# Kernel optimization log

Hardware: AMD Instinct MI355X
Metric: run time of the kernel (lower is better)

Reference implementation:

```python
import jax, jax.numpy as jnp
import numpy as np

D_MODEL = 1024
NUM_EXPERTS = 16
TOP_K = 2
CAPACITY_FACTOR = 1.25
SINKHORN_ITERS = 3
AUX_LOSS_WEIGHT = 0.01


def setup_inputs() -> dict:
    key = jax.random.key(0)
    ks = jax.random.split(key, 6)
    d, e, h = D_MODEL, NUM_EXPERTS, 4 * D_MODEL
    sd = 1.0 / np.sqrt(d)
    sh = 1.0 / np.sqrt(h)
    return {
        "x": jax.random.normal(ks[0], (4, 2048, d), dtype=jnp.float32),
        "W_router": jax.random.uniform(ks[1], (d, e), jnp.float32, -sd, sd),
        "W1": jax.random.uniform(ks[2], (e, d, h), jnp.float32, -sd, sd),
        "b1": jax.random.uniform(ks[3], (e, h), jnp.float32, -sd, sd),
        "W2": jax.random.uniform(ks[4], (e, h, d), jnp.float32, -sh, sh),
        "b2": jax.random.uniform(ks[5], (e, d), jnp.float32, -sh, sh),
    }


def _moe_forward(x, W_router, W1, b1, W2, b2):
    B, S, D = x.shape
    E, K = NUM_EXPERTS, TOP_K
    N = B * S
    capacity = max(int(N * CAPACITY_FACTOR / E), K)  # static python int

    xf = x.reshape(N, D)
    router_logits = xf @ W_router                      # [N, E]
    probs = jax.nn.softmax(router_logits, axis=-1)
    # Sinkhorn balancing (as in source: row-normalize, col-normalize, rescale)
    for _ in range(SINKHORN_ITERS):
        probs = probs / probs.sum(axis=-1, keepdims=True)
        probs = probs / probs.sum(axis=0, keepdims=True)
        probs = probs * (N / E)

    weights, indices = jax.lax.top_k(probs, K)         # [N, K]
    weights = weights / weights.sum(axis=-1, keepdims=True)

    # --- dispatch: sequential slot allocation in (t, k) order ---
    flat_e = indices.reshape(-1)                       # [N*K]
    onehot = (flat_e[:, None] == jnp.arange(E)[None, :]).astype(jnp.int32)  # [N*K, E]
    # position of each dispatch within its expert = count of earlier same-expert entries
    pos = (jnp.cumsum(onehot, axis=0) * onehot).sum(-1) - 1                  # [N*K]
    mask = pos < capacity                              # dispatch_mask flattened
    total_counts = onehot.sum(0)                       # [E]
    token_counts = jnp.minimum(total_counts, capacity)

    safe_pos = jnp.where(mask, pos, 0)
    flat_idx = jnp.where(mask, flat_e * capacity + safe_pos, E * capacity)
    x_rep = jnp.repeat(xf, K, axis=0)                  # [N*K, D], (t,k) order
    buf = jnp.zeros((E * capacity + 1, D), dtype=x.dtype)
    buf = buf.at[flat_idx].set(x_rep)
    expert_input = buf[: E * capacity].reshape(E, capacity, D)

    # --- per-expert MLP (exact GELU, as torch.nn.GELU default) ---
    h = jnp.einsum('ecd,edf->ecf', expert_input, W1) + b1[:, None, :]
    h = jax.nn.gelu(h, approximate=False)
    expert_output = jnp.einsum('ecf,efd->ecd', h, W2) + b2[:, None, :]  # [E, cap, D]

    # --- weighted gather-combine ---
    gathered = expert_output[flat_e, safe_pos]         # [N*K, D]
    w = (weights.reshape(-1) * mask.astype(weights.dtype))[:, None]
    y = (gathered * w).reshape(N, K, D).sum(axis=1).reshape(B, S, D)

    aux_loss = AUX_LOSS_WEIGHT * E * (
        probs.mean(axis=0) * (token_counts.astype(probs.dtype) / N)
    ).sum()
    return y, aux_loss


def reference(x, W_router, W1, b1, W2, b2):
    return _moe_forward(x, W_router, W1, b1, W2, b2)
```

## Files before the change

kernel.cpp:

```cpp
#include <hip/hip_runtime.h>
#include <hip/hip_bf16.h>
#include <math.h>

#define NTOK 8192
#define DM   1024
#define NE   16
#define HD   4096
#define CAP  640
#define NCHUNK 64

typedef float f32x4 __attribute__((ext_vector_type(4)));
typedef _Float16 f16x8 __attribute__((ext_vector_type(8)));
typedef _Float16 f16x4 __attribute__((ext_vector_type(4)));

__device__ __forceinline__ void gload16(const void* g, void* l) {
  __builtin_amdgcn_global_load_lds(
      (const __attribute__((address_space(1))) unsigned int*)g,
      (__attribute__((address_space(3))) unsigned int*)l, 16, 0, 0);
}

__device__ __forceinline__ float gelu_fast(float v) {
  float v2 = v * v;
  float z2n = v * fmaf(-0.07135481627f, v2, -1.595769122f);
  float e = __expf(z2n);
  return v / (1.0f + e);
}

__global__ __launch_bounds__(256) void k_router(const float* __restrict__ x,
                                                const float* __restrict__ Wr,
                                                float* __restrict__ probs,
                                                float* __restrict__ pout) {
  int wave = threadIdx.x >> 6, lane = threadIdx.x & 63;
  int tok = blockIdx.x * 4 + wave;
  const float* xr = x + (size_t)tok * DM;
  float acc[NE];
#pragma unroll
  for (int e = 0; e < NE; ++e) acc[e] = 0.f;
  for (int d = lane; d < DM; d += 64) {
    float xv = xr[d];
    const float* w = Wr + (size_t)d * NE;
#pragma unroll
    for (int e = 0; e < NE; ++e) acc[e] = fmaf(xv, w[e], acc[e]);
  }
#pragma unroll
  for (int off = 32; off >= 1; off >>= 1) {
#pragma unroll
    for (int e = 0; e < NE; ++e) acc[e] += __shfl_xor(acc[e], off, 64);
  }
  float m = acc[0];
#pragma unroll
  for (int e = 1; e < NE; ++e) m = fmaxf(m, acc[e]);
  float s = 0.f;
#pragma unroll
  for (int e = 0; e < NE; ++e) { acc[e] = expf(acc[e] - m); s += acc[e]; }
  float inv = 1.0f / s;
#pragma unroll
  for (int e = 0; e < NE; ++e) acc[e] *= inv;
  if (lane < NE) probs[(size_t)tok * NE + lane] = acc[lane];
  __shared__ float wsum[4][NE];
  if (lane == 0) {
#pragma unroll
    for (int e = 0; e < NE; ++e) wsum[wave][e] = acc[e];
  }
  __syncthreads();
  if (threadIdx.x < NE)
    pout[blockIdx.x * NE + threadIdx.x] =
        wsum[0][threadIdx.x] + wsum[1][threadIdx.x] + wsum[2][threadIdx.x] + wsum[3][threadIdx.x];
}

__global__ __launch_bounds__(256) void k_sink(float* __restrict__ probs,
                                              const float* __restrict__ pin,
                                              float* __restrict__ pout) {
  __shared__ float csinv[NE];
  int tid = threadIdx.x;
  if (tid < NE) {
    float s = 0.f;
#pragma unroll
    for (int b = 0; b < 32; ++b) s += pin[b * NE + tid];
    csinv[tid] = 512.0f / s;
  }
  __syncthreads();
  int tok = blockIdx.x * 256 + tid;
  float* row = probs + (size_t)tok * NE;
  float p[NE]; float rs = 0.f;
#pragma unroll
  for (int e = 0; e < NE; ++e) { p[e] = row[e] * csinv[e]; rs += p[e]; }
  float rinv = 1.0f / rs;
#pragma unroll
  for (int e = 0; e < NE; ++e) { p[e] *= rinv; row[e] = p[e]; }
#pragma unroll
  for (int off = 32; off >= 1; off >>= 1) {
#pragma unroll
    for (int e = 0; e < NE; ++e) p[e] += __shfl_xor(p[e], off, 64);
  }
  __shared__ float wsum[4][NE];
  int lane = tid & 63, wave = tid >> 6;
  if (lane == 0) {
#pragma unroll
    for (int e = 0; e < NE; ++e) wsum[wave][e] = p[e];
  }
  __syncthreads();
  if (tid < NE)
    pout[blockIdx.x * NE + tid] =
        wsum[0][tid] + wsum[1][tid] + wsum[2][tid] + wsum[3][tid];
}

__global__ __launch_bounds__(256) void k_sink3(const float* __restrict__ probs,
                                               const float* __restrict__ pin,
                                               int* __restrict__ eidx,
                                               float* __restrict__ ew,
                                               int* __restrict__ cnt) {
  __shared__ float csinv[NE];
  __shared__ int h0[NE], h1[NE];
  int tid = threadIdx.x;
  if (tid < NE) {
    float s = 0.f;
#pragma unroll
    for (int b = 0; b < 32; ++b) s += pin[b * NE + tid];
    csinv[tid] = 512.0f / s;
    h0[tid] = 0; h1[tid] = 0;
  }
  __syncthreads();
  int tok = blockIdx.x * 256 + tid;
  const float* row = probs + (size_t)tok * NE;
  float v0 = -1e30f, v1 = -1e30f; int e0 = 0, e1 = 0;
#pragma unroll
  for (int e = 0; e < NE; ++e) {
    float v = row[e] * csinv[e];
    if (v > v0) { v1 = v0; e1 = e0; v0 = v; e0 = e; }
    else if (v > v1) { v1 = v; e1 = e; }
  }
  float s = v0 + v1;
  eidx[tok * 2] = e0; eidx[tok * 2 + 1] = e1;
  ew[tok * 2] = v0 / s; ew[tok * 2 + 1] = v1 / s;
  int* hh = (tid < 128) ? h0 : h1;
  atomicAdd(&hh[e0], 1);
  atomicAdd(&hh[e1], 1);
  __syncthreads();
  if (tid < NE) cnt[(2 * blockIdx.x) * NE + tid] = h0[tid];
  else if (tid >= 32 && tid < 32 + NE) cnt[(2 * blockIdx.x + 1) * NE + (tid - 32)] = h1[tid - 32];
}

__global__ __launch_bounds__(64) void k_prefix(const int* __restrict__ cnt,
                                               int* __restrict__ base,
                                               int* __restrict__ counts,
                                               float* __restrict__ aux) {
  __shared__ int tot[NE];
  int e = threadIdx.x;
  if (e < NE) {
    int run = 0;
    for (int c = 0; c < NCHUNK; ++c) {
      base[c * NE + e] = run;
      run += cnt[c * NE + e];
    }
    counts[e] = run;
    tot[e] = min(run, CAP);
  }
  __syncthreads();
  if (e == 0) {
    int s = 0;
#pragma unroll
    for (int i = 0; i < NE; ++i) s += tot[i];
    *aux = 0.01f * (float)s / (float)NTOK;
  }
}

__global__ __launch_bounds__(256) void k_assign(const int* __restrict__ eidx,
                                                const int* __restrict__ base,
                                                int* __restrict__ slot_tok,
                                                int* __restrict__ tok2slot) {
  __shared__ int wcnt[4][NE];
  __shared__ int cbase[NE];
  int tid = threadIdx.x, c = blockIdx.x, lane = tid & 63, wave = tid >> 6;
  int i = c * 256 + tid;
  int myE = eidx[i];
  if (tid < NE) cbase[tid] = base[c * NE + tid];
  int mypre = 0;
#pragma unroll
  for (int e = 0; e < NE; ++e) {
    unsigned long long m = __ballot(myE == e);
    if (myE == e) mypre = __popcll(m & ((1ull << lane) - 1ull));
    if (lane == 0) wcnt[wave][e] = __popcll(m);
  }
  __syncthreads();
  int pre = 0;
  for (int w = 0; w < wave; ++w) pre += wcnt[w][myE];
  int pos = cbase[myE] + pre + mypre;
  if (pos < CAP) {
    slot_tok[myE * CAP + pos] = i >> 1;
    tok2slot[i] = myE * CAP + pos;
  } else {
    tok2slot[i] = -1;
  }
}

__global__ __launch_bounds__(256) void k_gather(const float* __restrict__ x,
                                                const int* __restrict__ slot_tok,
                                                _Float16* __restrict__ xg) {
  int row = blockIdx.x;
  int tok = slot_tok[row];
  int t = threadIdx.x;
  f16x4 h;
  if (tok >= 0) {
    float4 v = *(const float4*)(x + (size_t)tok * DM + t * 4);
    h[0] = (_Float16)v.x; h[1] = (_Float16)v.y; h[2] = (_Float16)v.z; h[3] = (_Float16)v.w;
  } else {
    h[0] = (_Float16)0.f; h[1] = (_Float16)0.f; h[2] = (_Float16)0.f; h[3] = (_Float16)0.f;
  }
  *(f16x4*)(xg + (size_t)row * DM + t * 4) = h;
}


__device__ __forceinline__ void stage_tileA128(const _Float16* gbase, int ld, int k0,
                                               _Float16* lds, int w, int lane) {
#pragma unroll
  for (int i = 0; i < 4; ++i) {
    int ci = (w * 4 + i) * 64 + lane;
    int row = ci >> 3, c = ci & 7;
    int cs = c ^ (row & 7);
    gload16(gbase + (size_t)row * ld + k0 + cs * 8, lds + (w * 4 + i) * 512);
  }
}

__device__ __forceinline__ void loadB8(const float* gb, int ld, int k0, int tid, float4* L) {
  int nq = tid & 31, kc = tid >> 5;
  const float* p = gb + (size_t)(k0 + kc * 8) * ld + nq * 4;
#pragma unroll
  for (int j = 0; j < 8; ++j) L[j] = *(const float4*)(p + (size_t)j * ld);
}

__device__ __forceinline__ void writeB(_Float16* Bs, int tid, const float4* L) {
  int nq = tid & 31, kc = tid >> 5;
#pragma unroll
  for (int i = 0; i < 4; ++i) {
    int n = nq * 4 + i;
    int pos = kc ^ ((n ^ (n >> 2)) & 7);
    f16x8 v;
#pragma unroll
    for (int j = 0; j < 8; ++j) {
      float f = (i == 0) ? L[j].x : (i == 1) ? L[j].y : (i == 2) ? L[j].z : L[j].w;
      v[j] = (_Float16)f;
    }
    *(f16x8*)(Bs + n * 64 + pos * 8) = v;
  }
}

#define MFMA_PHASE(Ac, Bs)                                                         \
  _Pragma("unroll")                                                                \
  for (int ks = 0; ks < 2; ++ks) {                                                 \
    f16x8 af[4], bf[4];                                                            \
    _Pragma("unroll")                                                              \
    for (int m = 0; m < 4; ++m) {                                                  \
      int row = wr * 64 + m * 16 + lr;                                             \
      int cs = (ks * 4 + kg) ^ (row & 7);                                          \
      af[m] = *(const f16x8*)((Ac) + row * 64 + cs * 8);                           \
    }                                                                              \
    _Pragma("unroll")                                                              \
    for (int n = 0; n < 4; ++n) {                                                  \
      int row = wc * 64 + n * 16 + lr;                                             \
      int cs = (ks * 4 + kg) ^ ((row ^ (row >> 2)) & 7);                           \
      bf[n] = *(const f16x8*)((Bs) + row * 64 + cs * 8);                           \
    }                                                                              \
    __builtin_amdgcn_s_setprio(1);                                                 \
    _Pragma("unroll")                                                              \
    for (int m = 0; m < 4; ++m)                                                    \
      _Pragma("unroll")                                                            \
      for (int n = 0; n < 4; ++n)                                                  \
        acc[m][n] = __builtin_amdgcn_mfma_f32_16x16x32_f16(af[m], bf[n], acc[m][n], 0, 0, 0); \
    __builtin_amdgcn_s_setprio(0);                                                 \
  }

#define ASYNC_K_LOOP(NT, AB, ALD, BB, BLD, KBASE)                                  \
  {                                                                                \
    stage_tileA128((AB), (ALD), (KBASE), As0, w, lane);                            \
    loadB8((BB), (BLD), (KBASE), tid, L);                                          \
    asm volatile("s_waitcnt vmcnt(0)" ::: "memory");                               \
    __builtin_amdgcn_s_barrier();                                                  \
    __builtin_amdgcn_sched_barrier(0);                                             \
    for (int t = 0; t < (NT); ++t) {                                               \
      const _Float16* Ac = (t & 1) ? As1 : As0;                                    \
      _Float16* An = (t & 1) ? As0 : As1;                                          \
      writeB(Bs, tid, L);                                                          \
      if (t + 1 < (NT)) {                                                          \
        stage_tileA128((AB), (ALD), (KBASE) + (t + 1) * 64, An, w, lane);          \
        loadB8((BB), (BLD), (KBASE) + (t + 1) * 64, tid, L);                       \
      }                                                                            \
      asm volatile("s_waitcnt lgkmcnt(0)" ::: "memory");                           \
      __builtin_amdgcn_s_barrier();                                                \
      __builtin_amdgcn_sched_barrier(0);                                           \
      MFMA_PHASE(Ac, Bs);                                                          \
      __builtin_amdgcn_sched_barrier(0);                                           \
      if (t + 1 < (NT)) { asm volatile("s_waitcnt vmcnt(8)" ::: "memory"); }       \
      else              { asm volatile("s_waitcnt vmcnt(0)" ::: "memory"); }       \
      __builtin_amdgcn_s_barrier();                                                \
      __builtin_amdgcn_sched_barrier(0);                                           \
    }                                                                              \
  }

__global__ __launch_bounds__(256) void k_gemm1(const _Float16* __restrict__ xg,
                                               const float* __restrict__ W1,
                                               const float* __restrict__ b1,
                                               _Float16* __restrict__ hbuf) {
  __shared__ _Float16 smem[3 * 128 * 64];
  _Float16* As0 = smem;
  _Float16* As1 = smem + 8192;
  _Float16* Bs  = smem + 16384;
  int bid = blockIdx.x;
  int logical = (bid & 7) * 320 + (bid >> 3);
  int my = logical % 5;
  int nx = (logical / 5) % 32;
  int e  = logical / 160;
  int m0 = my * 128, n0 = nx * 128;
  const _Float16* Ab = xg + ((size_t)e * CAP + m0) * DM;
  const float*    Bb = W1 + (size_t)e * DM * HD + n0;
  int tid = threadIdx.x, lane = tid & 63, w = tid >> 6;
  int wr = w >> 1, wc = w & 1;
  int lr = lane & 15, kg = lane >> 4;

  f32x4 acc[4][4];
#pragma unroll
  for (int m = 0; m < 4; ++m)
#pragma unroll
    for (int n = 0; n < 4; ++n) acc[m][n] = (f32x4){0.f, 0.f, 0.f, 0.f};

  float4 L[8];
  ASYNC_K_LOOP(16, Ab, DM, Bb, HD, 0);

  __syncthreads();
  _Float16* Cb = smem;
  int lq = lane >> 4;
#pragma unroll
  for (int n = 0; n < 4; ++n) {
    int col = wc * 64 + n * 16 + lr;
    float bias = b1[(size_t)e * HD + n0 + col];
#pragma unroll
    for (int m = 0; m < 4; ++m) {
#pragma unroll
      for (int r = 0; r < 4; ++r) {
        int row = wr * 64 + m * 16 + lq * 4 + r;
        float v = gelu_fast(acc[m][n][r] + bias);
        Cb[row * 128 + (col ^ (((row >> 2) & 3) << 4))] = (_Float16)v;
      }
    }
  }
  __syncthreads();
  int rr = tid >> 4;
  int c8 = (tid & 15) * 8;
#pragma unroll
  for (int p = 0; p < 8; ++p) {
    int row = p * 16 + rr;
    int colx = c8 ^ (((row >> 2) & 3) << 4);
    f16x8 v = *(const f16x8*)(Cb + row * 128 + colx);
    *(f16x8*)(hbuf + ((size_t)e * CAP + m0 + row) * HD + n0 + c8) = v;
  }
}

__global__ __launch_bounds__(256) void k_gemm2(const _Float16* __restrict__ hbuf,
                                               const float* __restrict__ W2,
                                               const float* __restrict__ b2,
                                               _Float16* __restrict__ P0,
                                               _Float16* __restrict__ P1) {
  __shared__ _Float16 smem[3 * 128 * 64];
  _Float16* As0 = smem;
  _Float16* As1 = smem + 8192;
  _Float16* Bs  = smem + 16384;
  int bid = blockIdx.x;
  int logical = (bid & 7) * 160 + (bid >> 3);
  int my = logical % 5;
  int nx = (logical / 5) % 8;
  int ks2 = (logical / 40) & 1;
  int e  = logical / 80;
  int m0 = my * 128, n0 = nx * 128, kbase = ks2 * 2048;
  const _Float16* Ab = hbuf + ((size_t)e * CAP + m0) * HD;
  const float*    Bb = W2 + (size_t)e * HD * DM + n0;
  int tid = threadIdx.x, lane = tid & 63, w = tid >> 6;
  int wr = w >> 1, wc = w & 1;
  int lr = lane & 15, kg = lane >> 4;

  f32x4 acc[4][4];
#pragma unroll
  for (int m = 0; m < 4; ++m)
#pragma unroll
    for (int n = 0; n < 4; ++n) acc[m][n] = (f32x4){0.f, 0.f, 0.f, 0.f};

  float4 L[8];
  ASYNC_K_LOOP(32, Ab, HD, Bb, DM, kbase);

  __syncthreads();
  _Float16* Cb = smem;
  _Float16* P = (ks2 == 0) ? P0 : P1;
  int lq = lane >> 4;
  float bias[4];
#pragma unroll
  for (int n = 0; n < 4; ++n)
    bias[n] = (ks2 == 0) ? b2[(size_t)e * DM + n0 + wc * 64 + n * 16 + lr] : 0.f;
#pragma unroll
  for (int m = 0; m < 4; ++m) {
#pragma unroll
    for (int n = 0; n < 4; ++n) {
#pragma unroll
      for (int r = 0; r < 4; ++r) {
        int row = wr * 64 + m * 16 + lq * 4 + r;
        int col = wc * 64 + n * 16 + lr;
        Cb[row * 128 + (col ^ (((row >> 2) & 3) << 4))] = (_Float16)(acc[m][n][r] + bias[n]);
      }
    }
  }
  __syncthreads();
  int rr = tid >> 4;
  int c8 = (tid & 15) * 8;
#pragma unroll
  for (int p = 0; p < 8; ++p) {
    int row = p * 16 + rr;
    int colx = c8 ^ (((row >> 2) & 3) << 4);
    f16x8 v = *(const f16x8*)(Cb + row * 128 + colx);
    *(f16x8*)(P + ((size_t)e * CAP + m0 + row) * DM + n0 + c8) = v;
  }
}

__global__ __launch_bounds__(256) void k_combine(const _Float16* __restrict__ P0,
                                                 const _Float16* __restrict__ P1,
                                                 const int* __restrict__ tok2slot,
                                                 const float* __restrict__ ew,
                                                 float* __restrict__ y) {
  int t = blockIdx.x;
  int d = threadIdx.x * 4;
  int i0 = tok2slot[t * 2], i1 = tok2slot[t * 2 + 1];
  float w0 = ew[t * 2], w1 = ew[t * 2 + 1];
  float a0 = 0.f, a1 = 0.f, a2 = 0.f, a3 = 0.f;
  if (i0 >= 0) {
    f16x4 oa = *(const f16x4*)(P0 + (size_t)i0 * DM + d);
    f16x4 ob = *(const f16x4*)(P1 + (size_t)i0 * DM + d);
    a0 += w0 * ((float)oa[0] + (float)ob[0]); a1 += w0 * ((float)oa[1] + (float)ob[1]);
    a2 += w0 * ((float)oa[2] + (float)ob[2]); a3 += w0 * ((float)oa[3] + (float)ob[3]);
  }
  if (i1 >= 0) {
    f16x4 oa = *(const f16x4*)(P0 + (size_t)i1 * DM + d);
    f16x4 ob = *(const f16x4*)(P1 + (size_t)i1 * DM + d);
    a0 += w1 * ((float)oa[0] + (float)ob[0]); a1 += w1 * ((float)oa[1] + (float)ob[1]);
    a2 += w1 * ((float)oa[2] + (float)ob[2]); a3 += w1 * ((float)oa[3] + (float)ob[3]);
  }
  float4 out = make_float4(a0, a1, a2, a3);
  *(float4*)(y + (size_t)t * DM + d) = out;
}

extern "C" void kernel_launch(void* const* d_in, const int* in_sizes, int n_in,
                              void* d_out, int out_size, void* d_ws, size_t ws_size,
                              hipStream_t stream) {
  const float* x  = (const float*)d_in[0];
  const float* Wr = (const float*)d_in[1];
  const float* W1 = (const float*)d_in[2];
  const float* b1 = (const float*)d_in[3];
  const float* W2 = (const float*)d_in[4];
  const float* b2 = (const float*)d_in[5];
  float* y = (float*)d_out;
  float* aux = y + (size_t)out_size - 1;

  char* ws = (char*)d_ws;
  float* probs    = (float*)ws; ws += (size_t)NTOK * NE * 4;
  float* C0       = (float*)ws; ws += 32 * NE * 4;
  float* C1       = (float*)ws; ws += 32 * NE * 4;
  int*   eidx     = (int*)ws;   ws += NTOK * 2 * 4;
  float* ew       = (float*)ws; ws += NTOK * 2 * 4;
  int*   slot_tok = (int*)ws;   ws += NE * CAP * 4;
  int*   tok2slot = (int*)ws;   ws += NTOK * 2 * 4;
  int*   counts   = (int*)ws;   ws += 256;
  int*   cnt      = (int*)ws;   ws += NCHUNK * NE * 4;
  int*   cbase    = (int*)ws;   ws += NCHUNK * NE * 4;
  _Float16* xg    = (_Float16*)ws; ws += (size_t)NE * CAP * DM * 2;
  _Float16* hbuf  = (_Float16*)ws; ws += (size_t)NE * CAP * HD * 2;
  _Float16* P1b   = (_Float16*)ws; ws += (size_t)NE * CAP * DM * 2;
  _Float16* P0b   = xg;

  hipMemsetAsync(slot_tok, 0xFF, (size_t)NE * CAP * 4, stream);

  k_router<<<NTOK / 4, 256, 0, stream>>>(x, Wr, probs, C0);
  k_sink<<<32, 256, 0, stream>>>(probs, C0, C1);
  k_sink<<<32, 256, 0, stream>>>(probs, C1, C0);
  k_sink3<<<32, 256, 0, stream>>>(probs, C0, eidx, ew, cnt);
  k_prefix<<<1, 64, 0, stream>>>(cnt, cbase, counts, aux);
  k_assign<<<NCHUNK, 256, 0, stream>>>(eidx, cbase, slot_tok, tok2slot);
  k_gather<<<NE * CAP, 256, 0, stream>>>(x, slot_tok, xg);

  k_gemm1<<<2560, 256, 0, stream>>>(xg, W1, b1, hbuf);
  k_gemm2<<<1280, 256, 0, stream>>>(hbuf, W2, b2, P0b, P1b);

  k_combine<<<NTOK, 256, 0, stream>>>(P0b, P1b, tok2slot, ew, y);
}
```

Before: 383.1 us.

## Widen GEMM1 tile to 256 rows so each W1 tile is reused twice

Rewrites the first expert GEMM kernel to compute 256x128 output tiles, with four waves each owning 64 rows by 128 columns. Each W1 fp32 tile is loaded and converted to fp16 once per 256 rows instead of once per 128, which halves the B-side global traffic and conversion work. Because 640 is not a multiple of 256, the last tile is padded: A-row addresses are clamped and out-of-range rows are skipped on store, so part of the MFMA work is wasted. The kernel now uses 80KB of dynamic shared memory and twice as many accumulators per thread, which may lower occupancy.

```diff
diff --git a/kernel.cpp b/kernel.cpp
--- a/kernel.cpp
+++ b/kernel.cpp
@@ -222,6 +222,18 @@
   }
 }
 
+__device__ __forceinline__ void stage_tileA128c(const _Float16* gbase, int ld, int k0,
+                                                _Float16* lds, int w, int lane, int al) {
+#pragma unroll
+  for (int i = 0; i < 4; ++i) {
+    int ci = (w * 4 + i) * 64 + lane;
+    int row = ci >> 3, c = ci & 7;
+    int cs = c ^ (row & 7);
+    int rc = row < al ? row : al;
+    gload16(gbase + (size_t)rc * ld + k0 + cs * 8, lds + (w * 4 + i) * 512);
+  }
+}
+
 __device__ __forceinline__ void loadB8(const float* gb, int ld, int k0, int tid, float4* L) {
   int nq = tid & 31, kc = tid >> 5;
   const float* p = gb + (size_t)(k0 + kc * 8) * ld + nq * 4;
@@ -242,6 +254,116 @@
       v[j] = (_Float16)f;
     }
     *(f16x8*)(Bs + n * 64 + pos * 8) = v;
+  }
+}
+
+__global__ __launch_bounds__(256) void k_gemm1(const _Float16* __restrict__ xg,
+                                               const float* __restrict__ W1,
+                                               const float* __restrict__ b1,
+                                               _Float16* __restrict__ hbuf) {
+  extern __shared__ _Float16 smem[];
+  _Float16* Bs = smem + 32768;
+  int bid = blockIdx.x;
+  int logical = (bid & 7) * 192 + (bid >> 3);
+  int mp = logical % 3;
+  int nx = (logical / 3) % 32;
+  int e  = logical / 96;
+  int m0 = mp * 256, n0 = nx * 128;
+  const _Float16* Aa = xg + ((size_t)e * CAP + m0) * DM;
+  const _Float16* Ab2 = xg + ((size_t)e * CAP + m0 + 128) * DM;
+  int alB = CAP - 1 - m0 - 128;
+  if (alB < 0) alB = 0;
+  if (alB > 127) alB = 127;
+  const float* Bb = W1 + (size_t)e * DM * HD + n0;
+  int tid = threadIdx.x, lane = tid & 63, w = tid >> 6;
+  int wh = w & 1;
+  int lr = lane & 15, kg = lane >> 4, lq = kg;
+
+  f32x4 acc[4][8];
+#pragma unroll
+  for (int m = 0; m < 4; ++m)
+#pragma unroll
+    for (int n = 0; n < 8; ++n) acc[m][n] = (f32x4){0.f, 0.f, 0.f, 0.f};
+
+  float4 L[8];
+  stage_tileA128(Aa, DM, 0, smem, w, lane);
+  stage_tileA128c(Ab2, DM, 0, smem + 8192, w, lane, alB);
+  loadB8(Bb, HD, 0, tid, L);
+  asm volatile("s_waitcnt vmcnt(0)" ::: "memory");
+  __builtin_amdgcn_s_barrier();
+  __builtin_amdgcn_sched_barrier(0);
+
+  for (int t = 0; t < 16; ++t) {
+    const _Float16* Ac = smem + ((t & 1) * 2 + (w >> 1)) * 8192;
+    _Float16* AnA = smem + (((t + 1) & 1) * 2 + 0) * 8192;
+    _Float16* AnB = smem + (((t + 1) & 1) * 2 + 1) * 8192;
+    writeB(Bs, tid, L);
+    if (t + 1 < 16) {
+      stage_tileA128(Aa, DM, (t + 1) * 64, AnA, w, lane);
+      stage_tileA128c(Ab2, DM, (t + 1) * 64, AnB, w, lane, alB);
+      __builtin_amdgcn_sched_barrier(0);
+      loadB8(Bb, HD, (t + 1) * 64, tid, L);
+    }
+    asm volatile("s_waitcnt lgkmcnt(0)" ::: "memory");
+    __builtin_amdgcn_s_barrier();
+    __builtin_amdgcn_sched_barrier(0);
+#pragma unroll
+    for (int ks = 0; ks < 2; ++ks) {
+      f16x8 af[4], bf[8];
+#pragma unroll
+      for (int m = 0; m < 4; ++m) {
+        int row = wh * 64 + m * 16 + lr;
+        int cs = (ks * 4 + kg) ^ (row & 7);
+        af[m] = *(const f16x8*)(Ac + row * 64 + cs * 8);
+      }
+#pragma unroll
+      for (int n = 0; n < 8; ++n) {
+        int row = n * 16 + lr;
+        int cs = (ks * 4 + kg) ^ ((row ^ (row >> 2)) & 7);
+        bf[n] = *(const f16x8*)(Bs + row * 64 + cs * 8);
+      }
+      __builtin_amdgcn_s_setprio(1);
+#pragma unroll
+      for (int m = 0; m < 4; ++m)
+#pragma unroll
+        for (int n = 0; n < 8; ++n)
+          acc[m][n] = __builtin_amdgcn_mfma_f32_16x16x32_f16(af[m], bf[n], acc[m][n], 0, 0, 0);
+      __builtin_amdgcn_s_setprio(0);
+    }
+    __builtin_amdgcn_sched_barrier(0);
+    if (t + 1 < 16) { asm volatile("s_waitcnt vmcnt(8)" ::: "memory"); }
+    else            { asm volatile("s_waitcnt vmcnt(0)" ::: "memory"); }
+    __builtin_amdgcn_s_barrier();
+    __builtin_amdgcn_sched_barrier(0);
+  }
+
+  __syncthreads();
+  _Float16* Cb = smem;
+#pragma unroll
+  for (int n = 0; n < 8; ++n) {
+    int col = n * 16 + lr;
+    float bias = b1[(size_t)e * HD + n0 + col];
+#pragma unroll
+    for (int m = 0; m < 4; ++m) {
+#pragma unroll
+      for (int r = 0; r < 4; ++r) {
+        int row = w * 64 + m * 16 + lq * 4 + r;
+        float v = gelu_fast(acc[m][n][r] + bias);
+        Cb[row * 128 + (col ^ (((row >> 2) & 3) << 4))] = (_Float16)v;
+      }
+    }
+  }
+  __syncthreads();
+  int rr = tid >> 4;
+  int c8 = (tid & 15) * 8;
+#pragma unroll
+  for (int p = 0; p < 16; ++p) {
+    int row = p * 16 + rr;
+    if (m0 + row < CAP) {
+      int colx = c8 ^ (((row >> 2) & 3) << 4);
+      f16x8 v = *(const f16x8*)(Cb + row * 128 + colx);
+      *(f16x8*)(hbuf + ((size_t)e * CAP + m0 + row) * HD + n0 + c8) = v;
+    }
   }
 }
 
@@ -297,64 +419,6 @@
     }                                                                              \
   }
 
-__global__ __launch_bounds__(256) void k_gemm1(const _Float16* __restrict__ xg,
-                                               const float* __restrict__ W1,
-                                               const float* __restrict__ b1,
-                                               _Float16* __restrict__ hbuf) {
-  __shared__ _Float16 smem[3 * 128 * 64];
-  _Float16* As0 = smem;
-  _Float16* As1 = smem + 8192;
-  _Float16* Bs  = smem + 16384;
-  int bid = blockIdx.x;
-  int logical = (bid & 7) * 320 + (bid >> 3);
-  int my = logical % 5;
-  int nx = (logical / 5) % 32;
-  int e  = logical / 160;
-  int m0 = my * 128, n0 = nx * 128;
-  const _Float16* Ab = xg + ((size_t)e * CAP + m0) * DM;
-  const float*    Bb = W1 + (size_t)e * DM * HD + n0;
-  int tid = threadIdx.x, lane = tid & 63, w = tid >> 6;
-  int wr = w >> 1, wc = w & 1;
-  int lr = lane & 15, kg = lane >> 4;
-
-  f32x4 acc[4][4];
-#pragma unroll
-  for (int m = 0; m < 4; ++m)
-#pragma unroll
-    for (int n = 0; n < 4; ++n) acc[m][n] = (f32x4){0.f, 0.f, 0.f, 0.f};
-
-  float4 L[8];
-  ASYNC_K_LOOP(16, Ab, DM, Bb, HD, 0);
-
-  __syncthreads();
-  _Float16* Cb = smem;
-  int lq = lane >> 4;
-#pragma unroll
-  for (int n = 0; n < 4; ++n) {
-    int col = wc * 64 + n * 16 + lr;
-    float bias = b1[(size_t)e * HD + n0 + col];
-#pragma unroll
-    for (int m = 0; m < 4; ++m) {
-#pragma unroll
-      for (int r = 0; r < 4; ++r) {
-        int row = wr * 64 + m * 16 + lq * 4 + r;
-        float v = gelu_fast(acc[m][n][r] + bias);
-        Cb[row * 128 + (col ^ (((row >> 2) & 3) << 4))] = (_Float16)v;
-      }
-    }
-  }
-  __syncthreads();
-  int rr = tid >> 4;
-  int c8 = (tid & 15) * 8;
-#pragma unroll
-  for (int p = 0; p < 8; ++p) {
-    int row = p * 16 + rr;
-    int colx = c8 ^ (((row >> 2) & 3) << 4);
-    f16x8 v = *(const f16x8*)(Cb + row * 128 + colx);
-    *(f16x8*)(hbuf + ((size_t)e * CAP + m0 + row) * HD + n0 + c8) = v;
-  }
-}
-
 __global__ __launch_bounds__(256) void k_gemm2(const _Float16* __restrict__ hbuf,
                                                const float* __restrict__ W2,
                                                const float* __restrict__ b2,
@@ -472,6 +536,8 @@
   _Float16* P1b   = (_Float16*)ws; ws += (size_t)NE * CAP * DM * 2;
   _Float16* P0b   = xg;
 
+  hipFuncSetAttribute((const void*)k_gemm1, hipFuncAttributeMaxDynamicSharedMemorySize, 81920);
+
   hipMemsetAsync(slot_tok, 0xFF, (size_t)NE * CAP * 4, stream);
 
   k_router<<<NTOK / 4, 256, 0, stream>>>(x, Wr, probs, C0);
@@ -482,7 +548,7 @@
   k_assign<<<NCHUNK, 256, 0, stream>>>(eidx, cbase, slot_tok, tok2slot);
   k_gather<<<NE * CAP, 256, 0, stream>>>(x, slot_tok, xg);
 
-  k_gemm1<<<2560, 256, 0, stream>>>(xg, W1, b1, hbuf);
+  k_gemm1<<<1536, 256, 81920, stream>>>(xg, W1, b1, hbuf);
   k_gemm2<<<1280, 256, 0, stream>>>(hbuf, W2, b2, P0b, P1b);
 
   k_combine<<<NTOK, 256, 0, stream>>>(P0b, P1b, tok2slot, ew, y);
```

After: 418.8 us. 9.3% more time.
